# Optimization experiments

Hardware: AMD Instinct MI355X
Metric: run time of the kernel (lower is better)

Reference implementation:

```python
import jax, jax.numpy as jnp
import numpy as np

B, S, D = 2, 2048, 1024
E, K = 8, 2
I = 938  # expert intermediate: _find_multiple(round(4*1024*2/3),256)//3 = 2816//3


def setup_inputs() -> dict:
    key = jax.random.key(0)
    ks = jax.random.split(key, 6)
    inv_sqrt_d = 1.0 / np.sqrt(D)
    inv_sqrt_i = 1.0 / np.sqrt(I)
    return {
        "hidden_states": jax.random.normal(ks[0], (B, S, D), jnp.float32),
        "gate_weight": jax.random.normal(ks[1], (E, D), jnp.float32) * inv_sqrt_d,
        "shared_gate_up": jax.random.normal(ks[2], (D, 2 * I), jnp.float32) * inv_sqrt_d,
        "shared_down": jax.random.normal(ks[3], (I, D), jnp.float32) * inv_sqrt_i,
        "expert_gate_up": jax.random.normal(ks[4], (E, D, 2 * I), jnp.float32) * inv_sqrt_d,
        "expert_down": jax.random.normal(ks[5], (E, I, D), jnp.float32) * inv_sqrt_i,
    }


def _swiglu(gu, w_down):
    gate, up = jnp.split(gu, 2, axis=-1)
    return (jax.nn.silu(gate) * up) @ w_down


def reference(hidden_states, gate_weight, shared_gate_up, shared_down,
              expert_gate_up, expert_down):
    b, s, d = hidden_states.shape
    x = hidden_states.reshape(-1, d)            # [T, D]
    T = x.shape[0]
    n_experts = gate_weight.shape[0]

    # shared expert (always active)
    out = _swiglu(x @ shared_gate_up, shared_down)

    # router: softmax in fp32, top-k, renormalize
    logits = x @ gate_weight.T                   # [T, E]
    probs = jax.nn.softmax(logits.astype(jnp.float32), axis=-1).astype(x.dtype)
    top_p, top_i = jax.lax.top_k(probs, K)       # [T, K]
    top_p = top_p / (top_p.sum(axis=-1, keepdims=True) + 1e-8)

    # dense combine weights: combine[t, e] = sum_k top_p[t,k] * [top_i[t,k]==e]
    combine = jnp.zeros((T, n_experts), x.dtype).at[
        jnp.arange(T)[:, None], top_i].add(top_p)

    # same math as per-token gathered bmm: sum_e combine[:,e] * expert_e(x)
    for e in range(n_experts):
        out = out + combine[:, e:e + 1] * _swiglu(x @ expert_gate_up[e], expert_down[e])

    return out.reshape(b, s, d)
```

## Files before the change

kernel.cpp:

```cpp
#include <hip/hip_runtime.h>
#include <hip/hip_bf16.h>
#include <stdint.h>

#define T_TOK 4096
#define D_DIM 1024
#define E_EXP 8
#define I_DIM 938
#define TWO_I 1876
#define NP2 2048
#define IP 1024

typedef __attribute__((ext_vector_type(8))) short bf16x8;
typedef __attribute__((ext_vector_type(4))) float f32x4;
typedef __attribute__((ext_vector_type(8))) unsigned short u16x8;
typedef __attribute__((ext_vector_type(4))) unsigned short u16x4;

static __device__ __forceinline__ unsigned short f2bf(float f) {
  union { float f; uint32_t u; } v; v.f = f;
  uint32_t r = v.u + 0x7fffu + ((v.u >> 16) & 1u);
  return (unsigned short)(r >> 16);
}
static __device__ __forceinline__ void gload16(const void* g, void* l) {
  __builtin_amdgcn_global_load_lds((__attribute__((address_space(1))) void*)g,
                                   (__attribute__((address_space(3))) void*)l, 16, 0, 0);
}

__global__ __launch_bounds__(256) void cvt_x_kernel(const float* __restrict__ x,
                                                    unsigned short* __restrict__ xb) {
  int i = blockIdx.x * 256 + threadIdx.x;
  float4 v = reinterpret_cast<const float4*>(x)[i];
  u16x4 o;
  o[0] = f2bf(v.x); o[1] = f2bf(v.y); o[2] = f2bf(v.z); o[3] = f2bf(v.w);
  reinterpret_cast<u16x4*>(xb)[i] = o;
}

__global__ __launch_bounds__(256) void router_kernel(const float* __restrict__ x,
                                                     const float* __restrict__ gw,
                                                     int* __restrict__ ti,
                                                     float* __restrict__ tw) {
  int t = blockIdx.x * 4 + (threadIdx.x >> 6);
  int lane = threadIdx.x & 63;
  const float* xp = x + (size_t)t * D_DIM;
  float xv[16];
  #pragma unroll
  for (int i = 0; i < 16; ++i) xv[i] = xp[lane + i * 64];
  float logit[E_EXP];
  #pragma unroll
  for (int e = 0; e < E_EXP; ++e) {
    const float* wp = gw + (size_t)e * D_DIM;
    float s = 0.f;
    #pragma unroll
    for (int i = 0; i < 16; ++i) s += xv[i] * wp[lane + i * 64];
    #pragma unroll
    for (int o = 32; o; o >>= 1) s += __shfl_xor(s, o);
    logit[e] = s;
  }
  float mx = logit[0];
  #pragma unroll
  for (int e = 1; e < E_EXP; ++e) mx = fmaxf(mx, logit[e]);
  float p[E_EXP], sum = 0.f;
  #pragma unroll
  for (int e = 0; e < E_EXP; ++e) { p[e] = __expf(logit[e] - mx); sum += p[e]; }
  int i1 = 0; float p1 = p[0];
  #pragma unroll
  for (int e = 1; e < E_EXP; ++e) if (p[e] > p1) { p1 = p[e]; i1 = e; }
  int i2 = -1; float p2 = -1.f;
  #pragma unroll
  for (int e = 0; e < E_EXP; ++e) if (e != i1 && p[e] > p2) { p2 = p[e]; i2 = e; }
  float P1 = p1 / sum, P2 = p2 / sum;
  float denom = P1 + P2 + 1e-8f;
  if (lane == 0) {
    ti[2 * t] = i1; ti[2 * t + 1] = i2;
    tw[2 * t] = P1 / denom; tw[2 * t + 1] = P2 / denom;
  }
}

__global__ void zero_cnt_kernel(int* cnt) { if (threadIdx.x < E_EXP) cnt[threadIdx.x] = 0; }

__global__ __launch_bounds__(256) void assign_kernel(const int* __restrict__ ti,
                                                     const float* __restrict__ tw,
                                                     int* __restrict__ cnt,
                                                     int* __restrict__ list,
                                                     float* __restrict__ wl, int cap) {
  int t = blockIdx.x * 256 + threadIdx.x;
  #pragma unroll
  for (int j = 0; j < 2; ++j) {
    int e = ti[2 * t + j];
    float w = tw[2 * t + j];
    int slot = atomicAdd(&cnt[e], 1);
    if (slot < cap) { list[e * cap + slot] = t; wl[e * cap + slot] = w; }
  }
}

__global__ __launch_bounds__(256) void transpose_gu_kernel(
    const float* __restrict__ sgu, const float* __restrict__ egu,
    unsigned short* __restrict__ wT) {
  int e = blockIdx.z;
  const float* w = (e == 0) ? sgu : egu + (size_t)(e - 1) * D_DIM * TWO_I;
  unsigned short* o = wT + (size_t)e * NP2 * D_DIM;
  int k0 = blockIdx.x * 64, n0 = blockIdx.y * 32;
  __shared__ unsigned short lds[32][72];
  int tid = threadIdx.x;
  int nn = tid & 31, kr = tid >> 5;
  int n = n0 + nn;
  int hc = n >> 1;
  int src = (hc < I_DIM) ? ((n & 1) ? (I_DIM + hc) : hc) : -1;
  #pragma unroll
  for (int i = 0; i < 8; ++i) {
    int k = k0 + kr + i * 8;
    float f = (src >= 0) ? w[(size_t)k * TWO_I + src] : 0.f;
    lds[nn][kr + i * 8] = f2bf(f);
  }
  __syncthreads();
  int nr = tid >> 3, kc = (tid & 7) * 8;
  u16x8 v;
  #pragma unroll
  for (int j = 0; j < 8; ++j) v[j] = lds[nr][kc + j];
  *reinterpret_cast<u16x8*>(&o[(size_t)(n0 + nr) * D_DIM + k0 + kc]) = v;
}

__global__ __launch_bounds__(256) void transpose_d_kernel(
    const float* __restrict__ sdn, const float* __restrict__ edn,
    unsigned short* __restrict__ wT) {
  int e = blockIdx.z;
  const float* w = (e == 0) ? sdn : edn + (size_t)(e - 1) * I_DIM * D_DIM;
  unsigned short* o = wT + (size_t)e * D_DIM * IP;
  int k0 = blockIdx.x * 64, n0 = blockIdx.y * 32;
  __shared__ unsigned short lds[32][72];
  int tid = threadIdx.x;
  int nn = tid & 31, kr = tid >> 5;
  #pragma unroll
  for (int i = 0; i < 8; ++i) {
    int k = k0 + kr + i * 8;
    float f = (k < I_DIM) ? w[(size_t)k * D_DIM + n0 + nn] : 0.f;
    lds[nn][kr + i * 8] = f2bf(f);
  }
  __syncthreads();
  int nr = tid >> 3, kc = (tid & 7) * 8;
  u16x8 v;
  #pragma unroll
  for (int j = 0; j < 8; ++j) v[j] = lds[nr][kc + j];
  *reinterpret_cast<u16x8*>(&o[(size_t)(n0 + nr) * IP + k0 + kc]) = v;
}

__global__ __launch_bounds__(512) void gemm1_kernel(
    const unsigned short* __restrict__ xb,
    const unsigned short* __restrict__ wTgu,
    unsigned short* __restrict__ h_sh,
    unsigned short* __restrict__ h_g,
    const int* __restrict__ list, const int* __restrict__ cnt, int cap) {
  const int orig = blockIdx.x;
  const int wg = (orig & 7) * (gridDim.x >> 3) + (orig >> 3);
  int e, mb, nb;
  if (wg < 128) { e = 0; mb = wg >> 3; nb = wg & 7; }
  else { int r = wg - 128; e = 1 + (r >> 6); int rem = r & 63; mb = rem >> 3; nb = rem & 7; }
  const int m0 = mb * 256, n0 = nb * 256;
  int count = T_TOK;
  unsigned short* h = h_sh;
  if (e > 0) {
    count = min(cnt[e - 1], cap);
    if (m0 >= count) return;
    h = h_g + (size_t)(e - 1) * cap * IP;
  }
  const unsigned short* w = wTgu + (size_t)e * NP2 * D_DIM;

  __shared__ __align__(16) unsigned short a_lds[256 * 64];
  __shared__ __align__(16) unsigned short b_lds[256 * 64];
  const int tid = threadIdx.x;
  const int wave = tid >> 6, lane = tid & 63;
  const int mw = (wave >> 2) * 128, nw = (wave & 3) * 64;
  const int fr = lane & 15, fq = lane >> 4;
  const int srow = tid >> 3;
  const int sk = (tid & 7) * 8;

  size_t arow[4], brow[4];
  #pragma unroll
  for (int c = 0; c < 4; ++c) {
    int rr = m0 + 64 * c + srow;
    if (e > 0) rr = list[(e - 1) * cap + min(rr, count - 1)];
    arow[c] = (size_t)rr * D_DIM;
    brow[c] = (size_t)(n0 + 64 * c + srow) * D_DIM;
  }

  f32x4 acc[8][4];
  #pragma unroll
  for (int m = 0; m < 8; ++m)
    #pragma unroll
    for (int n = 0; n < 4; ++n) acc[m][n] = (f32x4)0.f;

  for (int k0 = 0; k0 < D_DIM; k0 += 64) {
    __syncthreads();
    #pragma unroll
    for (int c = 0; c < 4; ++c) {
      gload16(xb + arow[c] + k0 + sk, &a_lds[(64 * c + srow) * 64 + sk]);
      gload16(w + brow[c] + k0 + sk, &b_lds[(64 * c + srow) * 64 + sk]);
    }
    __syncthreads();
    #pragma unroll
    for (int kk = 0; kk < 2; ++kk) {
      bf16x8 av[8], bv[4];
      #pragma unroll
      for (int m = 0; m < 8; ++m)
        av[m] = *reinterpret_cast<const bf16x8*>(&a_lds[(mw + m * 16 + fr) * 64 + kk * 32 + fq * 8]);
      #pragma unroll
      for (int n = 0; n < 4; ++n)
        bv[n] = *reinterpret_cast<const bf16x8*>(&b_lds[(nw + n * 16 + fr) * 64 + kk * 32 + fq * 8]);
      #pragma unroll
      for (int m = 0; m < 8; ++m)
        #pragma unroll
        for (int n = 0; n < 4; ++n)
          acc[m][n] = __builtin_amdgcn_mfma_f32_16x16x32_bf16(av[m], bv[n], acc[m][n], 0, 0, 0);
    }
  }
  const bool isGate = !(fr & 1);
  const int hcb = (n0 + nw) >> 1;
  #pragma unroll
  for (int m = 0; m < 8; ++m)
    #pragma unroll
    for (int n = 0; n < 4; ++n)
      #pragma unroll
      for (int q = 0; q < 4; ++q) {
        float v = acc[m][n][q];
        float pt = __shfl_xor(v, 1);
        if (isGate) {
          float hv = (v / (1.f + __expf(-v))) * pt;
          int trow = m0 + mw + m * 16 + fq * 4 + q;
          h[(size_t)trow * IP + hcb + n * 8 + (fr >> 1)] = f2bf(hv);
        }
      }
}

__global__ __launch_bounds__(512) void gemm2_kernel(
    const unsigned short* __restrict__ h_sh,
    const unsigned short* __restrict__ h_g,
    const unsigned short* __restrict__ wTd,
    float* __restrict__ out,
    const int* __restrict__ list, const float* __restrict__ wl,
    const int* __restrict__ cnt, int cap) {
  const int orig = blockIdx.x;
  const int wg = (orig & 7) * (gridDim.x >> 3) + (orig >> 3);
  int e, mb, nb;
  if (wg < 64) { e = -1; mb = wg >> 2; nb = wg & 3; }
  else { int r = wg - 64; e = r >> 5; int rem = r & 31; mb = rem >> 2; nb = rem & 3; }
  const int m0 = mb * 256, n0 = nb * 256;
  int count = T_TOK;
  const unsigned short* A = h_sh;
  if (e >= 0) {
    count = min(cnt[e], cap);
    if (m0 >= count) return;
    A = h_g + (size_t)e * cap * IP;
  }
  const unsigned short* B = wTd + (size_t)(e + 1) * D_DIM * IP;

  __shared__ __align__(16) unsigned short a_lds[256 * 64];
  __shared__ __align__(16) unsigned short b_lds[256 * 64];
  const int tid = threadIdx.x;
  const int wave = tid >> 6, lane = tid & 63;
  const int mw = (wave >> 2) * 128, nw = (wave & 3) * 64;
  const int fr = lane & 15, fq = lane >> 4;
  const int srow = tid >> 3;
  const int sk = (tid & 7) * 8;

  f32x4 acc[8][4];
  #pragma unroll
  for (int m = 0; m < 8; ++m)
    #pragma unroll
    for (int n = 0; n < 4; ++n) acc[m][n] = (f32x4)0.f;

  for (int k0 = 0; k0 < IP; k0 += 64) {
    __syncthreads();
    #pragma unroll
    for (int c = 0; c < 4; ++c) {
      gload16(A + (size_t)(m0 + 64 * c + srow) * IP + k0 + sk,
              &a_lds[(64 * c + srow) * 64 + sk]);
      gload16(B + (size_t)(n0 + 64 * c + srow) * IP + k0 + sk,
              &b_lds[(64 * c + srow) * 64 + sk]);
    }
    __syncthreads();
    #pragma unroll
    for (int kk = 0; kk < 2; ++kk) {
      bf16x8 av[8], bv[4];
      #pragma unroll
      for (int m = 0; m < 8; ++m)
        av[m] = *reinterpret_cast<const bf16x8*>(&a_lds[(mw + m * 16 + fr) * 64 + kk * 32 + fq * 8]);
      #pragma unroll
      for (int n = 0; n < 4; ++n)
        bv[n] = *reinterpret_cast<const bf16x8*>(&b_lds[(nw + n * 16 + fr) * 64 + kk * 32 + fq * 8]);
      #pragma unroll
      for (int m = 0; m < 8; ++m)
        #pragma unroll
        for (int n = 0; n < 4; ++n)
          acc[m][n] = __builtin_amdgcn_mfma_f32_16x16x32_bf16(av[m], bv[n], acc[m][n], 0, 0, 0);
    }
  }
  #pragma unroll
  for (int m = 0; m < 8; ++m)
    #pragma unroll
    for (int q = 0; q < 4; ++q) {
      int slot = m0 + mw + m * 16 + fq * 4 + q;
      if (slot < count) {
        int t = slot; float wgt = 1.f;
        if (e >= 0) { t = list[e * cap + slot]; wgt = wl[e * cap + slot]; }
        #pragma unroll
        for (int n = 0; n < 4; ++n)
          atomicAdd(&out[(size_t)t * D_DIM + n0 + nw + n * 16 + fr], wgt * acc[m][n][q]);
      }
    }
}

extern "C" void kernel_launch(void* const* d_in, const int* in_sizes, int n_in,
                              void* d_out, int out_size, void* d_ws, size_t ws_size,
                              hipStream_t stream) {
  const float* x   = (const float*)d_in[0];
  const float* gw  = (const float*)d_in[1];
  const float* sgu = (const float*)d_in[2];
  const float* sdn = (const float*)d_in[3];
  const float* egu = (const float*)d_in[4];
  const float* edn = (const float*)d_in[5];
  float* out = (float*)d_out;

  char* p = (char*)d_ws;
  unsigned short* xb   = (unsigned short*)p; p += (size_t)T_TOK * D_DIM * 2;
  unsigned short* wTgu = (unsigned short*)p; p += (size_t)9 * NP2 * D_DIM * 2;
  unsigned short* wTd  = (unsigned short*)p; p += (size_t)9 * D_DIM * IP * 2;
  unsigned short* h_sh = (unsigned short*)p; p += (size_t)T_TOK * IP * 2;

  size_t fixed_tail = (size_t)T_TOK * 2 * (4 + 4) + 64 + 256;
  size_t used = (size_t)(p - (char*)d_ws) + fixed_tail;
  size_t per_cap = (size_t)E_EXP * (IP * 2 + 4 + 4);
  long avail = (long)ws_size - (long)used;
  int cap = (int)(avail > 0 ? avail / (long)per_cap : 0);
  cap &= ~255;
  if (cap > 2048) cap = 2048;
  if (cap < 1536) cap = 1536;

  unsigned short* h_g = (unsigned short*)p; p += (size_t)E_EXP * cap * IP * 2;
  int*   ti   = (int*)p;   p += (size_t)T_TOK * 2 * 4;
  float* tw   = (float*)p; p += (size_t)T_TOK * 2 * 4;
  int*   list = (int*)p;   p += (size_t)E_EXP * cap * 4;
  float* wl   = (float*)p; p += (size_t)E_EXP * cap * 4;
  int*   cnt  = (int*)p;

  cvt_x_kernel<<<(T_TOK * D_DIM) / (4 * 256), 256, 0, stream>>>(x, xb);
  router_kernel<<<T_TOK / 4, 256, 0, stream>>>(x, gw, ti, tw);
  zero_cnt_kernel<<<1, 64, 0, stream>>>(cnt);
  assign_kernel<<<T_TOK / 256, 256, 0, stream>>>(ti, tw, cnt, list, wl, cap);
  transpose_gu_kernel<<<dim3(D_DIM / 64, NP2 / 32, 9), 256, 0, stream>>>(sgu, egu, wTgu);
  transpose_d_kernel<<<dim3(IP / 64, D_DIM / 32, 9), 256, 0, stream>>>(sdn, edn, wTd);
  hipMemsetAsync(d_out, 0, (size_t)out_size * 4, stream);

  gemm1_kernel<<<128 + E_EXP * 64, 512, 0, stream>>>(xb, wTgu, h_sh, h_g, list, cnt, cap);
  gemm2_kernel<<<64 + E_EXP * 32, 512, 0, stream>>>(h_sh, h_g, wTd, out, list, wl, cnt, cap);
}
```

Measured before the change: 505.2 us.

## Double-buffer GEMM LDS tiles and replace atomic scatter with a combine pass

Both GEMM kernels now use two LDS buffers so the global-to-LDS load of the next K tile is issued before the MFMAs on the current tile, dropping one barrier per iteration. The gemm2 epilogue no longer does fp32 atomicAdd into the output. It writes the shared-expert result directly and stores weighted per-expert rows into a new y_g buffer, and a new combine kernel gathers each token's two expert rows through recorded slot indices. This removes atomic contention and the output memset, at the cost of extra workspace and an extra fp32 round trip through memory. It also doubles LDS use to 128KB per block, which may reduce occupancy.

```diff
diff --git a/kernel.cpp b/kernel.cpp
--- a/kernel.cpp
+++ b/kernel.cpp
@@ -81,13 +81,15 @@
                                                      const float* __restrict__ tw,
                                                      int* __restrict__ cnt,
                                                      int* __restrict__ list,
-                                                     float* __restrict__ wl, int cap) {
+                                                     float* __restrict__ wl,
+                                                     int* __restrict__ sl, int cap) {
   int t = blockIdx.x * 256 + threadIdx.x;
   #pragma unroll
   for (int j = 0; j < 2; ++j) {
     int e = ti[2 * t + j];
     float w = tw[2 * t + j];
     int slot = atomicAdd(&cnt[e], 1);
+    sl[2 * t + j] = slot;
     if (slot < cap) { list[e * cap + slot] = t; wl[e * cap + slot] = w; }
   }
 }
@@ -164,8 +166,8 @@
   }
   const unsigned short* w = wTgu + (size_t)e * NP2 * D_DIM;
 
-  __shared__ __align__(16) unsigned short a_lds[256 * 64];
-  __shared__ __align__(16) unsigned short b_lds[256 * 64];
+  __shared__ __align__(16) unsigned short a_lds[2][256 * 64];
+  __shared__ __align__(16) unsigned short b_lds[2][256 * 64];
   const int tid = threadIdx.x;
   const int wave = tid >> 6, lane = tid & 63;
   const int mw = (wave >> 2) * 128, nw = (wave & 3) * 64;
@@ -188,29 +190,36 @@
     #pragma unroll
     for (int n = 0; n < 4; ++n) acc[m][n] = (f32x4)0.f;
 
-  for (int k0 = 0; k0 < D_DIM; k0 += 64) {
-    __syncthreads();
+  auto stage = [&](int buf, int k0) {
     #pragma unroll
     for (int c = 0; c < 4; ++c) {
-      gload16(xb + arow[c] + k0 + sk, &a_lds[(64 * c + srow) * 64 + sk]);
-      gload16(w + brow[c] + k0 + sk, &b_lds[(64 * c + srow) * 64 + sk]);
-    }
-    __syncthreads();
+      gload16(xb + arow[c] + k0 + sk, &a_lds[buf][(64 * c + srow) * 64 + sk]);
+      gload16(w + brow[c] + k0 + sk, &b_lds[buf][(64 * c + srow) * 64 + sk]);
+    }
+  };
+
+  stage(0, 0);
+  __syncthreads();
+  int cur = 0;
+  for (int t = 0; t < D_DIM / 64; ++t) {
+    if (t + 1 < D_DIM / 64) stage(cur ^ 1, (t + 1) * 64);
     #pragma unroll
     for (int kk = 0; kk < 2; ++kk) {
       bf16x8 av[8], bv[4];
       #pragma unroll
       for (int m = 0; m < 8; ++m)
-        av[m] = *reinterpret_cast<const bf16x8*>(&a_lds[(mw + m * 16 + fr) * 64 + kk * 32 + fq * 8]);
+        av[m] = *reinterpret_cast<const bf16x8*>(&a_lds[cur][(mw + m * 16 + fr) * 64 + kk * 32 + fq * 8]);
       #pragma unroll
       for (int n = 0; n < 4; ++n)
-        bv[n] = *reinterpret_cast<const bf16x8*>(&b_lds[(nw + n * 16 + fr) * 64 + kk * 32 + fq * 8]);
+        bv[n] = *reinterpret_cast<const bf16x8*>(&b_lds[cur][(nw + n * 16 + fr) * 64 + kk * 32 + fq * 8]);
       #pragma unroll
       for (int m = 0; m < 8; ++m)
         #pragma unroll
         for (int n = 0; n < 4; ++n)
           acc[m][n] = __builtin_amdgcn_mfma_f32_16x16x32_bf16(av[m], bv[n], acc[m][n], 0, 0, 0);
     }
+    __syncthreads();
+    cur ^= 1;
   }
   const bool isGate = !(fr & 1);
   const int hcb = (n0 + nw) >> 1;
@@ -234,9 +243,8 @@
     const unsigned short* __restrict__ h_sh,
     const unsigned short* __restrict__ h_g,
     const unsigned short* __restrict__ wTd,
-    float* __restrict__ out,
-    const int* __restrict__ list, const float* __restrict__ wl,
-    const int* __restrict__ cnt, int cap) {
+    float* __restrict__ out, float* __restrict__ y_g,
+    const float* __restrict__ wl, const int* __restrict__ cnt, int cap) {
   const int orig = blockIdx.x;
   const int wg = (orig & 7) * (gridDim.x >> 3) + (orig >> 3);
   int e, mb, nb;
@@ -252,8 +260,8 @@
   }
   const unsigned short* B = wTd + (size_t)(e + 1) * D_DIM * IP;
 
-  __shared__ __align__(16) unsigned short a_lds[256 * 64];
-  __shared__ __align__(16) unsigned short b_lds[256 * 64];
+  __shared__ __align__(16) unsigned short a_lds[2][256 * 64];
+  __shared__ __align__(16) unsigned short b_lds[2][256 * 64];
   const int tid = threadIdx.x;
   const int wave = tid >> 6, lane = tid & 63;
   const int mw = (wave >> 2) * 128, nw = (wave & 3) * 64;
@@ -267,31 +275,37 @@
     #pragma unroll
     for (int n = 0; n < 4; ++n) acc[m][n] = (f32x4)0.f;
 
-  for (int k0 = 0; k0 < IP; k0 += 64) {
-    __syncthreads();
+  auto stage = [&](int buf, int k0) {
     #pragma unroll
     for (int c = 0; c < 4; ++c) {
       gload16(A + (size_t)(m0 + 64 * c + srow) * IP + k0 + sk,
-              &a_lds[(64 * c + srow) * 64 + sk]);
+              &a_lds[buf][(64 * c + srow) * 64 + sk]);
       gload16(B + (size_t)(n0 + 64 * c + srow) * IP + k0 + sk,
-              &b_lds[(64 * c + srow) * 64 + sk]);
-    }
-    __syncthreads();
+              &b_lds[buf][(64 * c + srow) * 64 + sk]);
+    }
+  };
+  stage(0, 0);
+  __syncthreads();
+  int cur = 0;
+  for (int t = 0; t < IP / 64; ++t) {
+    if (t + 1 < IP / 64) stage(cur ^ 1, (t + 1) * 64);
     #pragma unroll
     for (int kk = 0; kk < 2; ++kk) {
       bf16x8 av[8], bv[4];
       #pragma unroll
       for (int m = 0; m < 8; ++m)
-        av[m] = *reinterpret_cast<const bf16x8*>(&a_lds[(mw + m * 16 + fr) * 64 + kk * 32 + fq * 8]);
+        av[m] = *reinterpret_cast<const bf16x8*>(&a_lds[cur][(mw + m * 16 + fr) * 64 + kk * 32 + fq * 8]);
       #pragma unroll
       for (int n = 0; n < 4; ++n)
-        bv[n] = *reinterpret_cast<const bf16x8*>(&b_lds[(nw + n * 16 + fr) * 64 + kk * 32 + fq * 8]);
+        bv[n] = *reinterpret_cast<const bf16x8*>(&b_lds[cur][(nw + n * 16 + fr) * 64 + kk * 32 + fq * 8]);
       #pragma unroll
       for (int m = 0; m < 8; ++m)
         #pragma unroll
         for (int n = 0; n < 4; ++n)
           acc[m][n] = __builtin_amdgcn_mfma_f32_16x16x32_bf16(av[m], bv[n], acc[m][n], 0, 0, 0);
     }
+    __syncthreads();
+    cur ^= 1;
   }
   #pragma unroll
   for (int m = 0; m < 8; ++m)
@@ -299,13 +313,36 @@
     for (int q = 0; q < 4; ++q) {
       int slot = m0 + mw + m * 16 + fq * 4 + q;
       if (slot < count) {
-        int t = slot; float wgt = 1.f;
-        if (e >= 0) { t = list[e * cap + slot]; wgt = wl[e * cap + slot]; }
-        #pragma unroll
-        for (int n = 0; n < 4; ++n)
-          atomicAdd(&out[(size_t)t * D_DIM + n0 + nw + n * 16 + fr], wgt * acc[m][n][q]);
+        if (e < 0) {
+          #pragma unroll
+          for (int n = 0; n < 4; ++n)
+            out[(size_t)slot * D_DIM + n0 + nw + n * 16 + fr] = acc[m][n][q];
+        } else {
+          float wgt = wl[e * cap + slot];
+          #pragma unroll
+          for (int n = 0; n < 4; ++n)
+            y_g[((size_t)e * cap + slot) * D_DIM + n0 + nw + n * 16 + fr] = wgt * acc[m][n][q];
+        }
       }
     }
+}
+
+__global__ __launch_bounds__(256) void combine_kernel(
+    float* __restrict__ out, const float* __restrict__ y_g,
+    const int* __restrict__ ti, const int* __restrict__ sl,
+    const int* __restrict__ cnt, int cap) {
+  int t = blockIdx.x;
+  int c = threadIdx.x * 4;
+  float4 v = *reinterpret_cast<float4*>(&out[(size_t)t * D_DIM + c]);
+  #pragma unroll
+  for (int j = 0; j < 2; ++j) {
+    int e = ti[2 * t + j], s = sl[2 * t + j];
+    if (s < cap) {
+      float4 y = *reinterpret_cast<const float4*>(&y_g[((size_t)e * cap + s) * D_DIM + c]);
+      v.x += y.x; v.y += y.y; v.z += y.z; v.w += y.w;
+    }
+  }
+  *reinterpret_cast<float4*>(&out[(size_t)t * D_DIM + c]) = v;
 }
 
 extern "C" void kernel_launch(void* const* d_in, const int* in_sizes, int n_in,
@@ -325,9 +362,9 @@
   unsigned short* wTd  = (unsigned short*)p; p += (size_t)9 * D_DIM * IP * 2;
   unsigned short* h_sh = (unsigned short*)p; p += (size_t)T_TOK * IP * 2;
 
-  size_t fixed_tail = (size_t)T_TOK * 2 * (4 + 4) + 64 + 256;
+  size_t fixed_tail = (size_t)T_TOK * 2 * (4 + 4 + 4) + 64 + 256;
   size_t used = (size_t)(p - (char*)d_ws) + fixed_tail;
-  size_t per_cap = (size_t)E_EXP * (IP * 2 + 4 + 4);
+  size_t per_cap = (size_t)E_EXP * (IP * 2 + D_DIM * 4 + 4 + 4);
   long avail = (long)ws_size - (long)used;
   int cap = (int)(avail > 0 ? avail / (long)per_cap : 0);
   cap &= ~255;
@@ -335,8 +372,10 @@
   if (cap < 1536) cap = 1536;
 
   unsigned short* h_g = (unsigned short*)p; p += (size_t)E_EXP * cap * IP * 2;
+  float* y_g  = (float*)p; p += (size_t)E_EXP * cap * D_DIM * 4;
   int*   ti   = (int*)p;   p += (size_t)T_TOK * 2 * 4;
   float* tw   = (float*)p; p += (size_t)T_TOK * 2 * 4;
+  int*   sl   = (int*)p;   p += (size_t)T_TOK * 2 * 4;
   int*   list = (int*)p;   p += (size_t)E_EXP * cap * 4;
   float* wl   = (float*)p; p += (size_t)E_EXP * cap * 4;
   int*   cnt  = (int*)p;
@@ -344,11 +383,11 @@
   cvt_x_kernel<<<(T_TOK * D_DIM) / (4 * 256), 256, 0, stream>>>(x, xb);
   router_kernel<<<T_TOK / 4, 256, 0, stream>>>(x, gw, ti, tw);
   zero_cnt_kernel<<<1, 64, 0, stream>>>(cnt);
-  assign_kernel<<<T_TOK / 256, 256, 0, stream>>>(ti, tw, cnt, list, wl, cap);
+  assign_kernel<<<T_TOK / 256, 256, 0, stream>>>(ti, tw, cnt, list, wl, sl, cap);
   transpose_gu_kernel<<<dim3(D_DIM / 64, NP2 / 32, 9), 256, 0, stream>>>(sgu, egu, wTgu);
   transpose_d_kernel<<<dim3(IP / 64, D_DIM / 32, 9), 256, 0, stream>>>(sdn, edn, wTd);
-  hipMemsetAsync(d_out, 0, (size_t)out_size * 4, stream);
 
   gemm1_kernel<<<128 + E_EXP * 64, 512, 0, stream>>>(xb, wTgu, h_sh, h_g, list, cnt, cap);
-  gemm2_kernel<<<64 + E_EXP * 32, 512, 0, stream>>>(h_sh, h_g, wTd, out, list, wl, cnt, cap);
-}
+  gemm2_kernel<<<64 + E_EXP * 32, 512, 0, stream>>>(h_sh, h_g, wTd, out, y_g, wl, cnt, cap);
+  combine_kernel<<<T_TOK, 256, 0, stream>>>(out, y_g, ti, sl, cnt, cap);
+}
```

Result: faster. 461.5 us (-8.7%).
